# Kernel optimization log

Measured on AMD Instinct MI355X. Metric: run time of the kernel, lower is better.

Reference implementation:

```python
import jax, jax.numpy as jnp
import numpy as np

B, N, E, C = 1, 100000, 1600000, 128


def setup_inputs() -> dict:
    key = jax.random.key(0)
    k1, k2, k3, k4 = jax.random.split(key, 4)
    x = jax.random.normal(k1, (B, N, C), dtype=jnp.float32)
    edge_index = jax.random.randint(k2, (2, E), 0, N, dtype=jnp.int32)
    W_2 = jax.random.normal(k3, (C,), dtype=jnp.float32)
    W_3 = jax.random.normal(k4, (C,), dtype=jnp.float32)
    return {"x": x, "edge_index": edge_index, "W_2": W_2, "W_3": W_3}


def reference(x, edge_index, W_2, W_3):
    # x: [B, N, C]; edge_index: [2, E] (src, dst)
    src, dst = edge_index[0], edge_index[1]
    num_nodes = x.shape[1]
    # per-edge attention weight: w[b,e] = <(x*W_3)[b,src_e], x[b,dst_e]>
    x3 = (x * W_3)[:, src, :]          # [B, E, C] gather
    x4 = x[:, dst, :]                  # [B, E, C] gather
    w = jnp.einsum('bec,bec->be', x3, x4)  # [B, E]
    # value messages with diagonal W_2 scaling, scattered to destination nodes.
    # Equivalent to out = einsum('bij,bih->bjh', dense_adj(w), x*W_2),
    # where dense_adj[src,dst] = w (to_dense_adj sums duplicate edges; so does segment_sum).
    x2 = x * W_2                       # [B, N, C]
    msg = w[..., None] * x2[:, src, :]  # [B, E, C]
    out = jax.vmap(lambda m: jax.ops.segment_sum(m, dst, num_segments=num_nodes))(msg)
    return out  # [B, N, C]
```

## Files before the change

kernel.cpp:

```cpp
#include <hip/hip_runtime.h>
#include <hip/hip_fp16.h>


#define CCH 128
#define BSHIFT 5
#define BWIDTH 32
#define MAXBIN 4096
#define CH 8192
#define LDSCAP 1280
#define TBINS 16
#define NBLKCAP 256


__global__ __launch_bounds__(256) void k_hist(
    const int* __restrict__ dst, int E, int NBIN, int* __restrict__ hist_bm)
{
    __shared__ int cnt[MAXBIN];
    const int blk = blockIdx.x;
    const int tid = threadIdx.x;
    for (int b = tid; b < NBIN; b += 256) cnt[b] = 0;
    __syncthreads();

    const int e0 = blk * CH;
    #pragma unroll
    for (int k = 0; k < CH / 1024; ++k) {
        const int g = (e0 >> 2) + k * 256 + tid;
        const int e = g << 2;
        if (e >= E) continue;
        if (e + 4 <= E) {
            const int4 d4 = reinterpret_cast<const int4*>(dst)[g];
            atomicAdd(&cnt[d4.x >> BSHIFT], 1);
            atomicAdd(&cnt[d4.y >> BSHIFT], 1);
            atomicAdd(&cnt[d4.z >> BSHIFT], 1);
            atomicAdd(&cnt[d4.w >> BSHIFT], 1);
        } else {
            for (int ee = e; ee < E; ++ee) atomicAdd(&cnt[dst[ee] >> BSHIFT], 1);
        }
    }
    __syncthreads();
    int* hb = hist_bm + (size_t)blk * NBIN;
    for (int b = tid; b < NBIN; b += 256) hb[b] = cnt[b];
}


__global__ __launch_bounds__(256) void k_pscan1(
    const int* __restrict__ hist_bm, int NBIN, int NBLK,
    int* __restrict__ partial, int* __restrict__ blocksum)
{
    __shared__ int tile[TBINS][NBLKCAP + 1];
    __shared__ int sdata[256];
    const int t = threadIdx.x;
    const int B0 = blockIdx.x * TBINS;

    for (int g = t; g < TBINS * (NBLKCAP + 1); g += 256)
        (&tile[0][0])[g] = 0;
    __syncthreads();

    for (int g = t; g < NBLK * TBINS; g += 256) {
        const int blk = g >> 4;
        const int tb  = g & (TBINS - 1);
        const int bin = B0 + tb;
        if (bin < NBIN) tile[tb][blk] = hist_bm[(size_t)blk * NBIN + bin];
    }
    __syncthreads();

    const int tb  = t >> 4;
    const int bk0 = (t & 15) * 16;
    int v[16];
    int local = 0;
    #pragma unroll
    for (int k = 0; k < 16; ++k) { v[k] = tile[tb][bk0 + k]; local += v[k]; }

    sdata[t] = local;
    __syncthreads();
    #pragma unroll
    for (int off = 1; off < 256; off <<= 1) {
        int val = (t >= off) ? sdata[t - off] : 0;
        __syncthreads();
        sdata[t] += val;
        __syncthreads();
    }
    const int incl = sdata[t];
    int run = incl - local;
    if (t == 255) blocksum[blockIdx.x] = incl;

    const int bin = B0 + tb;
    if (bin < NBIN) {
        #pragma unroll
        for (int k = 0; k < 16; ++k) {
            const int blk = bk0 + k;
            if (blk < NBLK) partial[(size_t)bin * NBLK + blk] = run;
            run += v[k];
        }
    }
}

__global__ void k_scan2(int* __restrict__ blocksum, int nb) {
    __shared__ int sdata[1024];
    const int t = threadIdx.x;
    const int v = (t < nb) ? blocksum[t] : 0;
    sdata[t] = v;
    __syncthreads();
    for (int off = 1; off < 1024; off <<= 1) {
        int val = (t >= off) ? sdata[t - off] : 0;
        __syncthreads();
        sdata[t] += val;
        __syncthreads();
    }
    if (t < nb) blocksum[t] = sdata[t] - v;
}


__global__ __launch_bounds__(256) void k_pack_place(
    const float* __restrict__ x, __half* __restrict__ xh, int n4,
    const int* __restrict__ src, const int* __restrict__ dst, int E,
    int NBIN, int NBLK,
    const int* __restrict__ partial, const int* __restrict__ blocksum,
    unsigned int* __restrict__ coarse)
{
    __shared__ int lcur[MAXBIN];
    const int tid = threadIdx.x;

    if (blockIdx.x >= (unsigned)NBLK) {
        const int i = (blockIdx.x - NBLK) * 256 + tid;
        if (i < n4) {
            float4 v = reinterpret_cast<const float4*>(x)[i];
            __half2* o = reinterpret_cast<__half2*>(xh) + (size_t)i * 2;
            o[0] = __floats2half2_rn(v.x, v.y);
            o[1] = __floats2half2_rn(v.z, v.w);
        }
        return;
    }

    const int blk = blockIdx.x;
    for (int b = tid; b < NBIN; b += 256) {
        lcur[b] = partial[(size_t)b * NBLK + blk] + blocksum[b / TBINS];
    }
    __syncthreads();

    const int e0 = blk * CH;
    #pragma unroll
    for (int k = 0; k < CH / 1024; ++k) {
        const int g = (e0 >> 2) + k * 256 + tid;
        const int e = g << 2;
        if (e >= E) continue;
        if (e + 4 <= E) {
            const int4 d4 = reinterpret_cast<const int4*>(dst)[g];
            const int4 s4 = reinterpret_cast<const int4*>(src)[g];
            int p;
            p = atomicAdd(&lcur[d4.x >> BSHIFT], 1);
            coarse[p] = (unsigned)s4.x | ((unsigned)(d4.x & (BWIDTH - 1)) << 17);
            p = atomicAdd(&lcur[d4.y >> BSHIFT], 1);
            coarse[p] = (unsigned)s4.y | ((unsigned)(d4.y & (BWIDTH - 1)) << 17);
            p = atomicAdd(&lcur[d4.z >> BSHIFT], 1);
            coarse[p] = (unsigned)s4.z | ((unsigned)(d4.z & (BWIDTH - 1)) << 17);
            p = atomicAdd(&lcur[d4.w >> BSHIFT], 1);
            coarse[p] = (unsigned)s4.w | ((unsigned)(d4.w & (BWIDTH - 1)) << 17);
        } else {
            for (int ee = e; ee < E; ++ee) {
                const int d = dst[ee], s = src[ee];
                int p = atomicAdd(&lcur[d >> BSHIFT], 1);
                coarse[p] = (unsigned)s | ((unsigned)(d & (BWIDTH - 1)) << 17);
            }
        }
    }
}


__global__ __launch_bounds__(256) void k_sort_accum(
    const __half* __restrict__ xh,
    const float* __restrict__ W2,
    const float* __restrict__ W3,
    const unsigned int* __restrict__ coarse,
    const int* __restrict__ partial, const int* __restrict__ blocksum,
    int NBIN, int NBLK, int E, int N,
    float* __restrict__ out)
{
    __shared__ unsigned int raw[LDSCAP];
    __shared__ int srcl[LDSCAP];
    __shared__ int cnt[BWIDTH], offs[BWIDTH], cur[BWIDTH];

    const int bin  = blockIdx.x;
    const int tid  = threadIdx.x;
    const int lane = tid & 63;
    const int grp  = lane >> 4;
    const int sl   = lane & 15;
    const int gid  = (tid >> 6) * 4 + grp;
    const int choff = sl << 4;
    const char* xb = (const char*)xh;

    union H { int4 i4; __half2 h[4]; };

    const int node0 = (bin << BSHIFT) + gid * 2;
    const int node1 = node0 + 1;
    H uD0, uD1;
    uD0.i4 = make_int4(0, 0, 0, 0);
    uD1.i4 = make_int4(0, 0, 0, 0);
    if (node0 < N) uD0.i4 = *reinterpret_cast<const int4*>(xb + (((size_t)node0) << 8) + choff);
    if (node1 < N) uD1.i4 = *reinterpret_cast<const int4*>(xb + (((size_t)node1) << 8) + choff);

    const size_t i0 = (size_t)bin * NBLK;
    const int beg = partial[i0] + blocksum[bin / TBINS];
    const int end = (bin + 1 < NBIN)
        ? partial[i0 + NBLK] + blocksum[(bin + 1) / TBINS] : E;
    const int mtot = end - beg;
    const int m = (mtot < LDSCAP) ? mtot : LDSCAP;

    if (tid < BWIDTH) cnt[tid] = 0;
    __syncthreads();

    for (int i = tid; i < m; i += 256) {
        unsigned u = coarse[beg + i];
        raw[i] = u;
        atomicAdd(&cnt[u >> 17], 1);
    }
    __syncthreads();

    if (tid < BWIDTH) {
        int c = cnt[tid];
        int v = c;
        #pragma unroll
        for (int d2 = 1; d2 < BWIDTH; d2 <<= 1) {
            int t2 = __shfl_up(v, d2, 64);
            if (tid >= d2) v += t2;
        }
        offs[tid] = v - c;
        cur[tid]  = v - c;
    }
    __syncthreads();

    for (int i = tid; i < m; i += 256) {
        const unsigned u = raw[i];
        const int p = atomicAdd(&cur[u >> 17], 1);
        srcl[p] = (int)(u & 0x1FFFFu);
    }
    __syncthreads();

    const float4 w3a = *reinterpret_cast<const float4*>(W3 + sl * 8);
    const float4 w3b = *reinterpret_cast<const float4*>(W3 + sl * 8 + 4);
    const float4 w2a = *reinterpret_cast<const float4*>(W2 + sl * 8);
    const float4 w2b = *reinterpret_cast<const float4*>(W2 + sl * 8 + 4);

    #pragma unroll
    for (int i = 0; i < 2; ++i) {
        const int node = (i == 0) ? node0 : node1;
        if (node >= N) continue;
        const int dl = gid * 2 + i;
        const H uD = (i == 0) ? uD0 : uD1;

        const float2 e0 = __half22float2(uD.h[0]);
        const float2 e1 = __half22float2(uD.h[1]);
        const float2 e2 = __half22float2(uD.h[2]);
        const float2 e3 = __half22float2(uD.h[3]);
        const float4 va = make_float4(w3a.x * e0.x, w3a.y * e0.y,
                                      w3a.z * e1.x, w3a.w * e1.y);
        const float4 vb = make_float4(w3b.x * e2.x, w3b.y * e2.y,
                                      w3b.z * e3.x, w3b.w * e3.y);

        float4 accA = make_float4(0.f, 0.f, 0.f, 0.f);
        float4 accB = make_float4(0.f, 0.f, 0.f, 0.f);

        const int b0 = offs[dl];
        const int c  = cnt[dl];

        int j = 0;
        for (; j + 4 <= c; j += 4) {
            const int s0 = srcl[b0 + j];
            const int s1 = srcl[b0 + j + 1];
            const int s2 = srcl[b0 + j + 2];
            const int s3 = srcl[b0 + j + 3];
            H u0, u1, u2, u3;
            u0.i4 = *reinterpret_cast<const int4*>(xb + (((size_t)s0) << 8) + choff);
            u1.i4 = *reinterpret_cast<const int4*>(xb + (((size_t)s1) << 8) + choff);
            u2.i4 = *reinterpret_cast<const int4*>(xb + (((size_t)s2) << 8) + choff);
            u3.i4 = *reinterpret_cast<const int4*>(xb + (((size_t)s3) << 8) + choff);
            const float2 f00 = __half22float2(u0.h[0]);
            const float2 f01 = __half22float2(u0.h[1]);
            const float2 f02 = __half22float2(u0.h[2]);
            const float2 f03 = __half22float2(u0.h[3]);
            const float2 f10 = __half22float2(u1.h[0]);
            const float2 f11 = __half22float2(u1.h[1]);
            const float2 f12 = __half22float2(u1.h[2]);
            const float2 f13 = __half22float2(u1.h[3]);
            const float2 f20 = __half22float2(u2.h[0]);
            const float2 f21 = __half22float2(u2.h[1]);
            const float2 f22 = __half22float2(u2.h[2]);
            const float2 f23 = __half22float2(u2.h[3]);
            const float2 f30 = __half22float2(u3.h[0]);
            const float2 f31 = __half22float2(u3.h[1]);
            const float2 f32 = __half22float2(u3.h[2]);
            const float2 f33 = __half22float2(u3.h[3]);
            float p0 = f00.x * va.x + f00.y * va.y + f01.x * va.z + f01.y * va.w
                     + f02.x * vb.x + f02.y * vb.y + f03.x * vb.z + f03.y * vb.w;
            float p1 = f10.x * va.x + f10.y * va.y + f11.x * va.z + f11.y * va.w
                     + f12.x * vb.x + f12.y * vb.y + f13.x * vb.z + f13.y * vb.w;
            float p2 = f20.x * va.x + f20.y * va.y + f21.x * va.z + f21.y * va.w
                     + f22.x * vb.x + f22.y * vb.y + f23.x * vb.z + f23.y * vb.w;
            float p3 = f30.x * va.x + f30.y * va.y + f31.x * va.z + f31.y * va.w
                     + f32.x * vb.x + f32.y * vb.y + f33.x * vb.z + f33.y * vb.w;
            #pragma unroll
            for (int off = 1; off < 16; off <<= 1) {
                p0 += __shfl_xor(p0, off, 64);
                p1 += __shfl_xor(p1, off, 64);
                p2 += __shfl_xor(p2, off, 64);
                p3 += __shfl_xor(p3, off, 64);
            }
            accA.x += p0 * f00.x + p1 * f10.x + p2 * f20.x + p3 * f30.x;
            accA.y += p0 * f00.y + p1 * f10.y + p2 * f20.y + p3 * f30.y;
            accA.z += p0 * f01.x + p1 * f11.x + p2 * f21.x + p3 * f31.x;
            accA.w += p0 * f01.y + p1 * f11.y + p2 * f21.y + p3 * f31.y;
            accB.x += p0 * f02.x + p1 * f12.x + p2 * f22.x + p3 * f32.x;
            accB.y += p0 * f02.y + p1 * f12.y + p2 * f22.y + p3 * f32.y;
            accB.z += p0 * f03.x + p1 * f13.x + p2 * f23.x + p3 * f33.x;
            accB.w += p0 * f03.y + p1 * f13.y + p2 * f23.y + p3 * f33.y;
        }
        for (; j < c; ++j) {
            H u0;
            u0.i4 = *reinterpret_cast<const int4*>(
                xb + (((size_t)srcl[b0 + j]) << 8) + choff);
            const float2 f0 = __half22float2(u0.h[0]);
            const float2 f1 = __half22float2(u0.h[1]);
            const float2 f2 = __half22float2(u0.h[2]);
            const float2 f3 = __half22float2(u0.h[3]);
            float p = f0.x * va.x + f0.y * va.y + f1.x * va.z + f1.y * va.w
                    + f2.x * vb.x + f2.y * vb.y + f3.x * vb.z + f3.y * vb.w;
            #pragma unroll
            for (int off = 1; off < 16; off <<= 1) p += __shfl_xor(p, off, 64);
            accA.x += p * f0.x; accA.y += p * f0.y;
            accA.z += p * f1.x; accA.w += p * f1.y;
            accB.x += p * f2.x; accB.y += p * f2.y;
            accB.z += p * f3.x; accB.w += p * f3.y;
        }
        for (int i2 = LDSCAP; i2 < mtot; ++i2) {
            const unsigned u = coarse[beg + i2];
            if ((int)(u >> 17) != dl) continue;
            H u0;
            u0.i4 = *reinterpret_cast<const int4*>(
                xb + (((size_t)(u & 0x1FFFFu)) << 8) + choff);
            const float2 f0 = __half22float2(u0.h[0]);
            const float2 f1 = __half22float2(u0.h[1]);
            const float2 f2 = __half22float2(u0.h[2]);
            const float2 f3 = __half22float2(u0.h[3]);
            float p = f0.x * va.x + f0.y * va.y + f1.x * va.z + f1.y * va.w
                    + f2.x * vb.x + f2.y * vb.y + f3.x * vb.z + f3.y * vb.w;
            #pragma unroll
            for (int off = 1; off < 16; off <<= 1) p += __shfl_xor(p, off, 64);
            accA.x += p * f0.x; accA.y += p * f0.y;
            accA.z += p * f1.x; accA.w += p * f1.y;
            accB.x += p * f2.x; accB.y += p * f2.y;
            accB.z += p * f3.x; accB.w += p * f3.y;
        }

        accA.x *= w2a.x; accA.y *= w2a.y; accA.z *= w2a.z; accA.w *= w2a.w;
        accB.x *= w2b.x; accB.y *= w2b.y; accB.z *= w2b.z; accB.w *= w2b.w;
        float* orow = out + (size_t)node * CCH + sl * 8;
        *reinterpret_cast<float4*>(orow)     = accA;
        *reinterpret_cast<float4*>(orow + 4) = accB;
    }
}


__global__ __launch_bounds__(256) void edge_gather_scatter(
    const float* __restrict__ x, const int* __restrict__ edge_index,
    const float* __restrict__ W2, const float* __restrict__ W3,
    float* __restrict__ out, int E)
{
    const int e    = (blockIdx.x * blockDim.x + threadIdx.x) >> 6;
    const int lane = threadIdx.x & 63;
    if (e >= E) return;
    const int s = edge_index[e];
    const int d = edge_index[E + e];
    const float2 xs = *reinterpret_cast<const float2*>(x + (size_t)s * CCH + lane * 2);
    const float2 xd = *reinterpret_cast<const float2*>(x + (size_t)d * CCH + lane * 2);
    const float2 w3 = *reinterpret_cast<const float2*>(W3 + lane * 2);
    const float2 w2 = *reinterpret_cast<const float2*>(W2 + lane * 2);
    float p = xs.x * w3.x * xd.x + xs.y * w3.y * xd.y;
    #pragma unroll
    for (int off = 32; off > 0; off >>= 1) p += __shfl_xor(p, off, 64);
    float* o = out + (size_t)d * CCH + lane * 2;
    atomicAdd(o,     p * xs.x * w2.x);
    atomicAdd(o + 1, p * xs.y * w2.y);
}


extern "C" void kernel_launch(void* const* d_in, const int* in_sizes, int n_in,
                              void* d_out, int out_size, void* d_ws, size_t ws_size,
                              hipStream_t stream) {
    const float* x          = (const float*)d_in[0];
    const int*   edge_index = (const int*)  d_in[1];
    const float* W2         = (const float*)d_in[2];
    const float* W3         = (const float*)d_in[3];
    float*       out        = (float*)d_out;

    const int E = in_sizes[1] / 2;
    const int N = out_size / CCH;
    const int* src = edge_index;
    const int* dst = edge_index + E;

    const int NBIN = (N + BWIDTH - 1) >> BSHIFT;
    const int NBLK = (E + CH - 1) / CH;
    const long long Mll = (long long)NBIN * NBLK;
    const int M = (int)Mll;
    const int nb1 = (NBIN + TBINS - 1) / TBINS;

    const size_t xh_bytes = (size_t)N * CCH * 2;
    const size_t need = xh_bytes + (size_t)E * 4 + 2 * (size_t)M * 4 + 1024 * 4;

    const bool aligned16 = (((uintptr_t)src & 15) == 0) && (((uintptr_t)dst & 15) == 0);

    if (N <= (1 << 17) && NBIN <= MAXBIN && NBLK <= NBLKCAP && Mll <= (1LL << 20) &&
        nb1 <= 1024 && aligned16 && ws_size >= need) {
        char* base = (char*)d_ws;
        __half* xh       = (__half*)base;        base += xh_bytes;
        unsigned* coarse = (unsigned*)base;      base += (size_t)E * 4;
        int* hist_bm     = (int*)base;           base += (size_t)M * 4;
        int* partial     = (int*)base;           base += (size_t)M * 4;
        int* blocksum    = (int*)base;

        const int n4 = N * CCH / 4;
        const int nPack = (n4 + 255) / 256;

        k_hist<<<NBLK, 256, 0, stream>>>(dst, E, NBIN, hist_bm);
        k_pscan1<<<nb1, 256, 0, stream>>>(hist_bm, NBIN, NBLK, partial, blocksum);
        k_scan2<<<1, 1024, 0, stream>>>(blocksum, nb1);
        k_pack_place<<<NBLK + nPack, 256, 0, stream>>>(x, xh, n4, src, dst, E,
                                                       NBIN, NBLK,
                                                       partial, blocksum, coarse);
        k_sort_accum<<<NBIN, 256, 0, stream>>>(xh, W2, W3, coarse,
                                               partial, blocksum,
                                               NBIN, NBLK, E, N, out);
        return;
    }

    hipMemsetAsync(d_out, 0, (size_t)out_size * sizeof(float), stream);
    const int grid = (E * 64 + 255) / 256;
    edge_gather_scatter<<<grid, 256, 0, stream>>>(x, edge_index, W2, W3, out, E);
}
```

Before: 126.9 us.

## Fold block-sum scan into consumers and spread fp16 packing across kernels

Removes the separate single-block scan kernel. Each block of the place kernel now recomputes the exclusive scan of block sums in LDS, and the accumulate kernel derives its two prefixes with a wavefront reduction. The fp32-to-fp16 packing of x is split into three parts and attached as extra blocks to the histogram, partial-scan and place kernels, so it runs alongside the low-occupancy stages. This saves one launch and fills idle CUs. In exchange every block does redundant scan work, and the path is limited to nb1 <= 256.

```diff
diff --git a/kernel.cpp b/kernel.cpp
--- a/kernel.cpp
+++ b/kernel.cpp
@@ -12,12 +12,32 @@
 #define NBLKCAP 256
 
 
-__global__ __launch_bounds__(256) void k_hist(
-    const int* __restrict__ dst, int E, int NBIN, int* __restrict__ hist_bm)
+__device__ __forceinline__ void pack_body(const float* __restrict__ x,
+                                          __half* __restrict__ xh,
+                                          int n4, int i) {
+    if (i < n4) {
+        float4 v = reinterpret_cast<const float4*>(x)[i];
+        __half2* o = reinterpret_cast<__half2*>(xh) + (size_t)i * 2;
+        o[0] = __floats2half2_rn(v.x, v.y);
+        o[1] = __floats2half2_rn(v.z, v.w);
+    }
+}
+
+
+__global__ __launch_bounds__(256) void k_hist_pack(
+    const int* __restrict__ dst, int E, int NBIN, int NBLK,
+    int* __restrict__ hist_bm,
+    const float* __restrict__ x, __half* __restrict__ xh, int n4, int pOff)
 {
     __shared__ int cnt[MAXBIN];
+    const int tid = threadIdx.x;
+
+    if ((int)blockIdx.x >= NBLK) {
+        pack_body(x, xh, n4, (pOff + (int)blockIdx.x - NBLK) * 256 + tid);
+        return;
+    }
+
     const int blk = blockIdx.x;
-    const int tid = threadIdx.x;
     for (int b = tid; b < NBIN; b += 256) cnt[b] = 0;
     __syncthreads();
 
@@ -43,13 +63,20 @@
 }
 
 
-__global__ __launch_bounds__(256) void k_pscan1(
-    const int* __restrict__ hist_bm, int NBIN, int NBLK,
-    int* __restrict__ partial, int* __restrict__ blocksum)
+__global__ __launch_bounds__(256) void k_pscan_pack(
+    const int* __restrict__ hist_bm, int NBIN, int NBLK, int nb1,
+    int* __restrict__ partial, int* __restrict__ blocksum,
+    const float* __restrict__ x, __half* __restrict__ xh, int n4, int pOff)
 {
     __shared__ int tile[TBINS][NBLKCAP + 1];
     __shared__ int sdata[256];
     const int t = threadIdx.x;
+
+    if ((int)blockIdx.x >= nb1) {
+        pack_body(x, xh, n4, (pOff + (int)blockIdx.x - nb1) * 256 + t);
+        return;
+    }
+
     const int B0 = blockIdx.x * TBINS;
 
     for (int g = t; g < TBINS * (NBLKCAP + 1); g += 256)
@@ -95,46 +122,40 @@
     }
 }
 
-__global__ void k_scan2(int* __restrict__ blocksum, int nb) {
-    __shared__ int sdata[1024];
-    const int t = threadIdx.x;
-    const int v = (t < nb) ? blocksum[t] : 0;
-    sdata[t] = v;
-    __syncthreads();
-    for (int off = 1; off < 1024; off <<= 1) {
-        int val = (t >= off) ? sdata[t - off] : 0;
-        __syncthreads();
-        sdata[t] += val;
-        __syncthreads();
-    }
-    if (t < nb) blocksum[t] = sdata[t] - v;
-}
-
-
-__global__ __launch_bounds__(256) void k_pack_place(
-    const float* __restrict__ x, __half* __restrict__ xh, int n4,
+
+__global__ __launch_bounds__(256) void k_place_pack(
     const int* __restrict__ src, const int* __restrict__ dst, int E,
-    int NBIN, int NBLK,
+    int NBIN, int NBLK, int nb1,
     const int* __restrict__ partial, const int* __restrict__ blocksum,
-    unsigned int* __restrict__ coarse)
+    unsigned int* __restrict__ coarse,
+    const float* __restrict__ x, __half* __restrict__ xh, int n4, int pOff)
 {
     __shared__ int lcur[MAXBIN];
+    __shared__ int sdata[256];
+    __shared__ int sblk[256];
     const int tid = threadIdx.x;
 
-    if (blockIdx.x >= (unsigned)NBLK) {
-        const int i = (blockIdx.x - NBLK) * 256 + tid;
-        if (i < n4) {
-            float4 v = reinterpret_cast<const float4*>(x)[i];
-            __half2* o = reinterpret_cast<__half2*>(xh) + (size_t)i * 2;
-            o[0] = __floats2half2_rn(v.x, v.y);
-            o[1] = __floats2half2_rn(v.z, v.w);
-        }
+    if ((int)blockIdx.x >= NBLK) {
+        pack_body(x, xh, n4, (pOff + (int)blockIdx.x - NBLK) * 256 + tid);
         return;
     }
+
+    sdata[tid] = (tid < nb1) ? blocksum[tid] : 0;
+    const int own = sdata[tid];
+    __syncthreads();
+    #pragma unroll
+    for (int off = 1; off < 256; off <<= 1) {
+        int val = (tid >= off) ? sdata[tid - off] : 0;
+        __syncthreads();
+        sdata[tid] += val;
+        __syncthreads();
+    }
+    sblk[tid] = sdata[tid] - own;
+    __syncthreads();
 
     const int blk = blockIdx.x;
     for (int b = tid; b < NBIN; b += 256) {
-        lcur[b] = partial[(size_t)b * NBLK + blk] + blocksum[b / TBINS];
+        lcur[b] = partial[(size_t)b * NBLK + blk] + sblk[b / TBINS];
     }
     __syncthreads();
 
@@ -173,7 +194,7 @@
     const float* __restrict__ W3,
     const unsigned int* __restrict__ coarse,
     const int* __restrict__ partial, const int* __restrict__ blocksum,
-    int NBIN, int NBLK, int E, int N,
+    int NBIN, int NBLK, int nb1, int E, int N,
     float* __restrict__ out)
 {
     __shared__ unsigned int raw[LDSCAP];
@@ -199,10 +220,22 @@
     if (node0 < N) uD0.i4 = *reinterpret_cast<const int4*>(xb + (((size_t)node0) << 8) + choff);
     if (node1 < N) uD1.i4 = *reinterpret_cast<const int4*>(xb + (((size_t)node1) << 8) + choff);
 
+    const int j1 = bin / TBINS;
+    const int j2 = (bin + 1) / TBINS;
+    int s = 0;
+    #pragma unroll
+    for (int k = 0; k < 4; ++k) {
+        const int idx = lane + k * 64;
+        if (idx < j1) s += blocksum[idx];
+    }
+    #pragma unroll
+    for (int off = 32; off > 0; off >>= 1) s += __shfl_xor(s, off, 64);
+    const int pref1 = s;
+    const int pref2 = pref1 + ((j2 > j1 && j2 <= nb1) ? blocksum[j1] : 0);
+
     const size_t i0 = (size_t)bin * NBLK;
-    const int beg = partial[i0] + blocksum[bin / TBINS];
-    const int end = (bin + 1 < NBIN)
-        ? partial[i0 + NBLK] + blocksum[(bin + 1) / TBINS] : E;
+    const int beg = partial[i0] + pref1;
+    const int end = (bin + 1 < NBIN) ? partial[i0 + NBLK] + pref2 : E;
     const int mtot = end - beg;
     const int m = (mtot < LDSCAP) ? mtot : LDSCAP;
 
@@ -409,7 +442,7 @@
     const bool aligned16 = (((uintptr_t)src & 15) == 0) && (((uintptr_t)dst & 15) == 0);
 
     if (N <= (1 << 17) && NBIN <= MAXBIN && NBLK <= NBLKCAP && Mll <= (1LL << 20) &&
-        nb1 <= 1024 && aligned16 && ws_size >= need) {
+        nb1 <= 256 && aligned16 && ws_size >= need) {
         char* base = (char*)d_ws;
         __half* xh       = (__half*)base;        base += xh_bytes;
         unsigned* coarse = (unsigned*)base;      base += (size_t)E * 4;
@@ -419,16 +452,21 @@
 
         const int n4 = N * CCH / 4;
         const int nPack = (n4 + 255) / 256;
-
-        k_hist<<<NBLK, 256, 0, stream>>>(dst, E, NBIN, hist_bm);
-        k_pscan1<<<nb1, 256, 0, stream>>>(hist_bm, NBIN, NBLK, partial, blocksum);
-        k_scan2<<<1, 1024, 0, stream>>>(blocksum, nb1);
-        k_pack_place<<<NBLK + nPack, 256, 0, stream>>>(x, xh, n4, src, dst, E,
-                                                       NBIN, NBLK,
-                                                       partial, blocksum, coarse);
+        const int nP1 = (nPack + 2) / 3;
+        const int nP2 = (nPack + 2) / 3;
+        const int nP3 = nPack - nP1 - nP2;
+
+        k_hist_pack<<<NBLK + nP1, 256, 0, stream>>>(dst, E, NBIN, NBLK, hist_bm,
+                                                    x, xh, n4, 0);
+        k_pscan_pack<<<nb1 + nP2, 256, 0, stream>>>(hist_bm, NBIN, NBLK, nb1,
+                                                    partial, blocksum,
+                                                    x, xh, n4, nP1);
+        k_place_pack<<<NBLK + nP3, 256, 0, stream>>>(src, dst, E, NBIN, NBLK, nb1,
+                                                     partial, blocksum, coarse,
+                                                     x, xh, n4, nP1 + nP2);
         k_sort_accum<<<NBIN, 256, 0, stream>>>(xh, W2, W3, coarse,
                                                partial, blocksum,
-                                               NBIN, NBLK, E, N, out);
+                                               NBIN, NBLK, nb1, E, N, out);
         return;
     }
 
```

After: 124.0 us. 2.3% less time.
